# Performance work log

Hardware: AMD Instinct MI355X
Metric: run time of the kernel (lower is better)

The kernel has to match this reference:

```python
import jax, jax.numpy as jnp
import numpy as np

DIM = 192; HEADS = 6; WS = 8; OVERLAP = 2; PAD = 3; STRIDE = WS - OVERLAP; HID = DIM * 4

_coords = np.stack(np.meshgrid(np.arange(WS), np.arange(WS), indexing='ij'), 0).reshape(2, -1)
_rel = (_coords[:, :, None] - _coords[:, None, :]).transpose(1, 2, 0).astype(np.int64)
_rel[..., 0] += WS - 1; _rel[..., 1] += WS - 1; _rel[..., 0] *= 2 * WS - 1
REL_IDX = jnp.asarray(_rel.sum(-1).reshape(-1))  # (WS^2 * WS^2,)


def _ln_c(x, g, b):
    # LayerNorm over channel dim of NCHW (LayerNormProxy)
    mu = jnp.mean(x, axis=1, keepdims=True)
    var = jnp.mean((x - mu) ** 2, axis=1, keepdims=True)
    return (x - mu) * jax.lax.rsqrt(var + 1e-5) * g[:, None, None] + b[:, None, None]


def _conv1x1(x, w, b):
    return jnp.einsum('bchw,oc->bohw', x, w) + b[:, None, None]


def _dwconv3(x, w, b):
    y = jax.lax.conv_general_dilated(x, w, (1, 1), ((1, 1), (1, 1)),
                                     feature_group_count=x.shape[1],
                                     dimension_numbers=('NCHW', 'OIHW', 'NCHW'))
    return y + b[:, None, None]


def _unfold(x, k, s, p):
    # F.unfold: (B,C,H,W) -> (B, C*k*k, L) with (C,kh,kw) channel order, row-major windows
    B, C, H, W = x.shape
    xp = jnp.pad(x, ((0, 0), (0, 0), (p, p), (p, p)))
    Lh = (H + 2 * p - k) // s + 1; Lw = (W + 2 * p - k) // s + 1
    ih = (jnp.arange(Lh) * s)[:, None] + jnp.arange(k)  # (Lh,k)
    iw = (jnp.arange(Lw) * s)[:, None] + jnp.arange(k)  # (Lw,k)
    t = xp[:, :, ih, :][:, :, :, :, iw]                 # (B,C,Lh,k,Lw,k)
    t = t.transpose(0, 1, 3, 5, 2, 4)                   # (B,C,k,k,Lh,Lw)
    return t.reshape(B, C * k * k, Lh * Lw)


def _fold(cols, h, w, k, s, p):
    # F.fold: (B, C*k*k, L) -> (B,C,h,w), summing overlaps
    B = cols.shape[0]
    Lh = (h + 2 * p - k) // s + 1; Lw = (w + 2 * p - k) // s + 1
    C = cols.shape[1] // (k * k)
    t = cols.reshape(B, C, k, k, Lh, Lw).transpose(0, 1, 4, 2, 5, 3)  # (B,C,Lh,k,Lw,k)
    ih = (jnp.arange(Lh) * s)[:, None] + jnp.arange(k)
    iw = (jnp.arange(Lw) * s)[:, None] + jnp.arange(k)
    out = jnp.zeros((B, C, h + 2 * p, w + 2 * p), cols.dtype)
    out = out.at[:, :, ih[:, :, None, None], iw[None, None, :, :]].add(t)
    return out[:, :, p:p + h, p:p + w]


def _reverse(win, h, w):
    B, L, nH, ws2, ch = win.shape
    cols = win.transpose(0, 2, 4, 3, 1).reshape(B, nH * ch * ws2, L)
    return _fold(cols, h, w, WS, STRIDE, PAD)


def _hft(x, w, b):
    # HFTAttention: high-frequency residual of multi-scale avg pools, dw-conv sigmoid gate
    B, C, h, ww = x.shape
    a = 3.0 * x
    for s in (2, 4, 8):
        pool = x.reshape(B, C, h // s, s, ww // s, s).mean(axis=(3, 5))
        a = a - jnp.repeat(jnp.repeat(pool, s, axis=2), s, axis=3)
    return jax.nn.sigmoid(_dwconv3(a, w, b)) * x


def _forward(x, n1g, n1b, qkv_w, qkv_b, temp, rpb, proj_w, proj_b, hft_w, hft_b,
             n2g, n2b, fc1_w, fc1_b, sgn_g, sgn_b, sg_w, sg_b, fc2_w, fc2_b):
    B, C, H, W = x.shape
    ch = C // HEADS
    y = _conv1x1(_ln_c(x, n1g, n1b), qkv_w, qkv_b)       # (B,3C,H,W)
    cols = _unfold(y, WS, STRIDE, PAD)
    L = cols.shape[-1]
    win = cols.reshape(B, 3 * HEADS, ch, WS * WS, L).transpose(0, 4, 1, 3, 2)  # (B,L,3H,ws2,ch)
    q = win[:, :, :HEADS] * temp[None, None]
    k = win[:, :, HEADS:2 * HEADS]
    v = win[:, :, 2 * HEADS:]
    attn = jnp.einsum('blhic,blhjc->blhij', q, k)
    bias = rpb[REL_IDX].reshape(WS * WS, WS * WS, HEADS).transpose(2, 0, 1)
    attn = attn + bias[None, None]
    e = jnp.exp(attn - jnp.max(attn, axis=-1, keepdims=True))
    s = jnp.sum(e, axis=-1, keepdims=True)               # (B,L,H,ws2,1)
    s_img = _reverse(s, H, W)                            # (B,HEADS,H,W): folded softmax denom
    o = jnp.einsum('blhij,blhjc->blhic', e, v)
    o_img = _reverse(o, H, W).reshape(B, HEADS, ch, H, W)
    out = (o_img / s_img[:, :, None]).reshape(B, C, H, W)
    out = _hft(_conv1x1(out, proj_w, proj_b), hft_w, hft_b)
    x1 = x + out
    z = jax.nn.gelu(_conv1x1(_ln_c(x1, n2g, n2b), fc1_w, fc1_b), approximate=False)
    z1, z2 = jnp.split(z, 2, axis=1)
    z = z1 * _dwconv3(_ln_c(z2, sgn_g, sgn_b), sg_w, sg_b)
    return x1 + _conv1x1(z, fc2_w, fc2_b)


def setup_inputs() -> dict:
    key = jax.random.key(0)
    ks = jax.random.split(key, 8)
    B, Hi, Wi = 4, 128, 128
    f = jnp.float32
    return {
        'x': jax.random.normal(ks[0], (B, DIM, Hi, Wi), f),
        'n1g': jnp.ones((DIM,), f), 'n1b': jnp.zeros((DIM,), f),
        'qkv_w': jax.random.normal(ks[1], (3 * DIM, DIM), f) * 0.02,
        'qkv_b': jnp.zeros((3 * DIM,), f),
        'temp': jnp.ones((HEADS, 1, 1), f),
        'rpb': jax.random.normal(ks[2], ((2 * WS - 1) ** 2, HEADS), f) * 0.02,
        'proj_w': jax.random.normal(ks[3], (DIM, DIM), f) * 0.02,
        'proj_b': jnp.zeros((DIM,), f),
        'hft_w': jax.random.normal(ks[4], (DIM, 1, 3, 3), f) * 0.02,
        'hft_b': jnp.zeros((DIM,), f),
        'n2g': jnp.ones((DIM,), f), 'n2b': jnp.zeros((DIM,), f),
        'fc1_w': jax.random.normal(ks[5], (HID, DIM), f) * 0.02,
        'fc1_b': jnp.zeros((HID,), f),
        'sgn_g': jnp.ones((HID // 2,), f), 'sgn_b': jnp.zeros((HID // 2,), f),
        'sg_w': jax.random.normal(ks[6], (HID // 2, 1, 3, 3), f) * 0.02,
        'sg_b': jnp.zeros((HID // 2,), f),
        'fc2_w': jax.random.normal(ks[7], (DIM, HID // 2), f) * 0.02,
        'fc2_b': jnp.zeros((DIM,), f),
    }


def reference(x, n1g, n1b, qkv_w, qkv_b, temp, rpb, proj_w, proj_b, hft_w, hft_b,
              n2g, n2b, fc1_w, fc1_b, sgn_g, sgn_b, sg_w, sg_b, fc2_w, fc2_b):
    return _forward(x, n1g, n1b, qkv_w, qkv_b, temp, rpb, proj_w, proj_b, hft_w, hft_b,
                    n2g, n2b, fc1_w, fc1_b, sgn_g, sgn_b, sg_w, sg_b, fc2_w, fc2_b)
```

## Files before the change

kernel.cpp:

```cpp
#include <hip/hip_runtime.h>
#include <math.h>

static constexpr int B_    = 4;
static constexpr int C_    = 192;
static constexpr int NPIX  = 16384;
static constexpr int PTOT  = B_ * NPIX;
static constexpr int HEADS = 6;
static constexpr int STR   = 6;
static constexpr int LH    = 22;
static constexpr int LWIN  = LH * LH;
static constexpr int NWIN  = B_ * LWIN;

typedef short bf16x8 __attribute__((ext_vector_type(8)));
typedef float f32x4  __attribute__((ext_vector_type(4)));

__device__ __forceinline__ unsigned short f2bf(float f) {
    union { float f; unsigned int u; } v; v.f = f;
    return (unsigned short)((v.u + 0x8000u) >> 16);
}
__device__ __forceinline__ float bf2f(unsigned short h) {
    union { unsigned int u; float f; } v; v.u = ((unsigned int)h) << 16;
    return v.f;
}
__device__ __forceinline__ unsigned int pack2bf(float a, float b) {
    union { float f; unsigned int u; } x, y; x.f = a; y.f = b;
    return __builtin_amdgcn_perm(y.u + 0x8000u, x.u + 0x8000u, 0x07060302u);
}
__device__ __forceinline__ float gelu_f(float v) {
    float vv = v * v;
    float u  = v * fmaf(vv, 0.0713548162f, 1.5957691216f);
    float ue = (u > 80.f) ? 80.f : u;
    float e  = __expf(ue);
    float r  = __builtin_amdgcn_rcpf(e + 1.f);
    return v * e * r;
}

__global__ __launch_bounds__(256) void prep_k(const float* __restrict__ W, const float* __restrict__ g,
                                              const float* __restrict__ bln, const float* __restrict__ bias,
                                              int M, int K,
                                              unsigned short* __restrict__ wgb, float* __restrict__ wsum,
                                              float* __restrict__ wb) {
    int o = blockIdx.x * 256 + threadIdx.x;
    if (o >= M) return;
    float sum = 0.f, bb = 0.f;
    for (int c = 0; c < K; ++c) {
        float wv = W[(size_t)o * K + c];
        float wgv = wv * g[c];
        wgb[(size_t)o * K + c] = f2bf(wgv);
        sum += wgv;
        bb += wv * bln[c];
    }
    wsum[o] = sum;
    wb[o] = bb + bias[o];
}

__global__ __launch_bounds__(256) void wcvt_k(const float* __restrict__ W, unsigned short* __restrict__ Wb, int n) {
    int i = blockIdx.x * 256 + threadIdx.x;
    if (i < n) Wb[i] = f2bf(W[i]);
}

__global__ __launch_bounds__(256) void lnstats_z2_k(const unsigned short* __restrict__ z,
                                                    float* __restrict__ mu, float* __restrict__ rs) {
    __shared__ float red[2][4][64];
    int n0 = blockIdx.x << 6, b = blockIdx.y;
    int t = threadIdx.x;
    int px = n0 + (t & 63), cg = t >> 6;
    float s = 0.f, s2 = 0.f;
    for (int c = cg; c < 384; c += 4) {
        float v = bf2f(z[((size_t)(b * 768 + 384 + c) << 14) + px]);
        s += v; s2 += v * v;
    }
    red[0][cg][t & 63] = s;
    red[1][cg][t & 63] = s2;
    __syncthreads();
    if (t < 64) {
        float ss  = red[0][0][t] + red[0][1][t] + red[0][2][t] + red[0][3][t];
        float ss2 = red[1][0][t] + red[1][1][t] + red[1][2][t] + red[1][3][t];
        float m = ss * (1.f / 384.f);
        mu[(b << 14) + n0 + t] = m;
        rs[(b << 14) + n0 + t] = rsqrtf(ss2 * (1.f / 384.f) - m * m + 1e-5f);
    }
}

template <int KK, int INMODE, int MPB, int ACT, bool LN, bool RES, bool OBF>
__global__ __launch_bounds__(256) void gemm4_k(const unsigned short* __restrict__ Wb,
                                               const void* __restrict__ Xin,
                                               void* __restrict__ outv,
                                               const float* __restrict__ wsum, const float* __restrict__ wb,
                                               const float* __restrict__ resid, int M, int bstride) {
    constexpr int LDK     = KK + 8;
    constexpr int KSTEPS  = KK / 32;
    constexpr int PFG     = (KSTEPS > 6) ? 6 : KSTEPS;
    __shared__ unsigned short xs[64 * LDK];
    __shared__ float sred[2][4][64];
    __shared__ float muL[64], rsL[64];

    int t = threadIdx.x;
    int pt = blockIdx.x;
    int b  = pt >> 8;
    int n0 = (pt & 255) << 6;

    if constexpr (INMODE == 0) {
        const unsigned short* xg = (const unsigned short*)Xin + (size_t)(b * NPIX + n0) * KK;
        constexpr int NJ = KK / 8;
        #pragma unroll
        for (int i = 0; i < 64 * NJ / 256; ++i) {
            int c = i * 256 + t;
            int p, j;
            if (KK == 192) { p = (c * 2731) >> 16; j = c - p * 24; }
            else           { int q = c >> 4; p = (q * 21846) >> 16; j = c - p * 48; }
            uint4 v = *(const uint4*)(xg + (size_t)c * 8);
            *(uint4*)&xs[p * LDK + j * 8] = v;
        }
    } else if constexpr (INMODE == 1) {
        const float* xg = (const float*)Xin + (size_t)b * bstride + n0;
        int px = t & 63, c0 = t >> 6;
        float s = 0.f, s2 = 0.f;
        #pragma unroll 4
        for (int st = 0; st < KK / 4; ++st) {
            int c = c0 + 4 * st;
            float v = xg[(size_t)c * NPIX + px];
            s += v; s2 += v * v;
            xs[px * LDK + c] = f2bf(v);
        }
        sred[0][c0][px] = s;
        sred[1][c0][px] = s2;
        __syncthreads();
        if (t < 64) {
            float ss  = sred[0][0][t] + sred[0][1][t] + sred[0][2][t] + sred[0][3][t];
            float ss2 = sred[1][0][t] + sred[1][1][t] + sred[1][2][t] + sred[1][3][t];
            float m = ss * (1.f / (float)KK);
            muL[t] = m;
            rsL[t] = rsqrtf(ss2 * (1.f / (float)KK) - m * m + 1e-5f);
        }
    } else {
        const unsigned short* xg = (const unsigned short*)Xin + (size_t)b * bstride + n0;
        int px2 = (t & 31) << 1, c0 = t >> 5;
        #pragma unroll 4
        for (int st = 0; st < KK / 8; ++st) {
            int c = c0 + 8 * st;
            unsigned int v = *(const unsigned int*)(xg + (size_t)c * NPIX + px2);
            xs[px2 * LDK + c]       = (unsigned short)(v & 0xFFFFu);
            xs[(px2 + 1) * LDK + c] = (unsigned short)(v >> 16);
        }
    }
    __syncthreads();

    int w  = t >> 6, l = t & 63;
    int wr = w >> 1, wc = w & 1;
    int lr = l & 15, kb = l >> 4;
    int pw = wr * 32;

    bf16x8 afr[KSTEPS][2];
    #pragma unroll
    for (int ks = 0; ks < KSTEPS; ++ks)
        #pragma unroll
        for (int m = 0; m < 2; ++m)
            afr[ks][m] = *(const bf16x8*)&xs[(pw + m * 16 + lr) * LDK + ks * 32 + kb * 8];

    float rsv[2][4], murs[2][4];
    if (LN) {
        #pragma unroll
        for (int m = 0; m < 2; ++m) {
            int pl = pw + m * 16 + kb * 4;
            #pragma unroll
            for (int r = 0; r < 4; ++r) {
                float mv = muL[pl + r];
                rsv[m][r] = rsL[pl + r];
                murs[m][r] = mv * rsv[m][r];
            }
        }
    }

    int ocbase = blockIdx.y * MPB;
    #pragma unroll 2
    for (int oc = 0; oc < MPB; ++oc) {
        int ow = ((ocbase + oc) << 6) + wc * 32;
        f32x4 acc[2][2];
        #pragma unroll
        for (int m = 0; m < 2; ++m)
            #pragma unroll
            for (int n = 0; n < 2; ++n) acc[m][n] = (f32x4){0.f, 0.f, 0.f, 0.f};

        #pragma unroll
        for (int kg = 0; kg < KSTEPS; kg += PFG) {
            bf16x8 bfr[PFG][2];
            #pragma unroll
            for (int kk = 0; kk < PFG; ++kk)
                #pragma unroll
                for (int n = 0; n < 2; ++n)
                    bfr[kk][n] = *(const bf16x8*)(Wb + (size_t)(ow + n * 16 + lr) * KK + (kg + kk) * 32 + kb * 8);
            #pragma unroll
            for (int kk = 0; kk < PFG; ++kk)
                #pragma unroll
                for (int m = 0; m < 2; ++m)
                    #pragma unroll
                    for (int n = 0; n < 2; ++n)
                        acc[m][n] = __builtin_amdgcn_mfma_f32_16x16x32_bf16(afr[kg + kk][m], bfr[kk][n], acc[m][n], 0, 0, 0);
        }

        #pragma unroll
        for (int m = 0; m < 2; ++m) {
            int nidx = n0 + pw + m * 16 + kb * 4;
            #pragma unroll
            for (int n = 0; n < 2; ++n) {
                int o = ow + n * 16 + lr;
                float wbv = wb[o];
                float wsv = 0.f; if (LN) wsv = wsum[o];
                size_t obase = (((size_t)b * M + o) << 14) + nidx;
                float rv[4] = {0.f, 0.f, 0.f, 0.f};
                if (RES) {
                    float4 rr = *(const float4*)(resid + obase);
                    rv[0] = rr.x; rv[1] = rr.y; rv[2] = rr.z; rv[3] = rr.w;
                }
                float vo[4];
                #pragma unroll
                for (int r = 0; r < 4; ++r) {
                    float a = acc[m][n][r];
                    float v;
                    if (LN) { float t1 = fmaf(-murs[m][r], wsv, wbv); v = fmaf(rsv[m][r], a, t1); }
                    else    v = a + wbv;
                    if (ACT == 1) v = gelu_f(v);
                    vo[r] = v + rv[r];
                }
                if (OBF) {
                    uint2 u;
                    u.x = pack2bf(vo[0], vo[1]);
                    u.y = pack2bf(vo[2], vo[3]);
                    *(uint2*)((unsigned short*)outv + obase) = u;
                } else {
                    float4 f = {vo[0], vo[1], vo[2], vo[3]};
                    *(float4*)((float*)outv + obase) = f;
                }
            }
        }
    }
}

__global__ __launch_bounds__(64) void attn_mfma_k(const unsigned short* __restrict__ qkv,
                                                  const float* __restrict__ rpb,
                                                  const float* __restrict__ temp,
                                                  unsigned short* __restrict__ o_win,
                                                  float* __restrict__ s_win) {
    __shared__ unsigned short p_lds[64 * 72];
    __shared__ float rp[225];
    int wh = blockIdx.x;
    int head = wh % HEADS;
    int bw = wh / HEADS;
    int b = bw / LWIN, l = bw % LWIN;
    int sh = l / LH, sw = l % LH;
    int h0 = sh * STR - 3, w0 = sw * STR - 3;
    int t = threadIdx.x;
    int lr = t & 15, kb = t >> 4;

    for (int i = t; i < 225; i += 64) rp[i] = rpb[i * HEADS + head];
    float tmp = temp[head];

    const size_t qbase = ((size_t)(b * 576 + head * 32)) << 14;
    const unsigned short* qp = qkv + qbase;
    const unsigned short* kp = qkv + qbase + ((size_t)192 << 14);
    const unsigned short* vp = qkv + qbase + ((size_t)384 << 14);

    bf16x8 kf[4], qf[4];
    #pragma unroll
    for (int m = 0; m < 4; ++m) {
        int jp = m * 16 + lr;
        int hh = h0 + (jp >> 3), ww = w0 + (jp & 7);
        bool ok = ((unsigned)hh < 128u) && ((unsigned)ww < 128u);
        int pix = (hh << 7) + ww;
        #pragma unroll
        for (int j = 0; j < 8; ++j) {
            unsigned short kv = 0, qv = 0;
            if (ok) {
                size_t off = ((size_t)(kb * 8 + j) << 14) + pix;
                kv = kp[off];
                qv = qp[off];
            }
            kf[m][j] = (short)kv;
            qf[m][j] = (short)qv;
        }
    }

    f32x4 st[4][4];
    #pragma unroll
    for (int m = 0; m < 4; ++m)
        #pragma unroll
        for (int n = 0; n < 4; ++n) st[m][n] = (f32x4){0.f, 0.f, 0.f, 0.f};
    #pragma unroll
    for (int m = 0; m < 4; ++m)
        #pragma unroll
        for (int n = 0; n < 4; ++n)
            st[m][n] = __builtin_amdgcn_mfma_f32_16x16x32_bf16(kf[m], qf[n], st[m][n], 0, 0, 0);

    bf16x8 vf[2][2];
    #pragma unroll
    for (int np = 0; np < 2; ++np) {
        #pragma unroll
        for (int ks = 0; ks < 2; ++ks) {
            int hh = h0 + ks * 4 + kb;
            bool okr = (unsigned)hh < 128u;
            const unsigned short* vrow = vp + (((size_t)(np * 16 + lr)) << 14) + (hh << 7) + w0;
            #pragma unroll
            for (int j = 0; j < 8; ++j) {
                int ww = w0 + j;
                unsigned short vv = 0;
                if (okr && (unsigned)ww < 128u) vv = vrow[j];
                vf[np][ks][j] = (short)vv;
            }
        }
    }

    __syncthreads();

    #pragma unroll
    for (int n = 0; n < 4; ++n) {
        int i = n * 16 + lr;
        int iyy = i >> 3, ixx = i & 7;
        #pragma unroll
        for (int m = 0; m < 4; ++m) {
            #pragma unroll
            for (int r = 0; r < 4; ++r) {
                int j = m * 16 + kb * 4 + r;
                int dy = iyy - (j >> 3) + 7;
                int dx = ixx - (j & 7) + 7;
                st[m][n][r] = st[m][n][r] * tmp + rp[dy * 15 + dx];
            }
        }
    }

    #pragma unroll
    for (int n = 0; n < 4; ++n) {
        float mx = -1e30f;
        #pragma unroll
        for (int m = 0; m < 4; ++m)
            #pragma unroll
            for (int r = 0; r < 4; ++r) mx = fmaxf(mx, st[m][n][r]);
        mx = fmaxf(mx, __shfl_xor(mx, 16));
        mx = fmaxf(mx, __shfl_xor(mx, 32));
        float s = 0.f;
        #pragma unroll
        for (int m = 0; m < 4; ++m) {
            #pragma unroll
            for (int r = 0; r < 4; ++r) {
                float e = __expf(st[m][n][r] - mx);
                st[m][n][r] = e;
                s += e;
            }
        }
        s += __shfl_xor(s, 16);
        s += __shfl_xor(s, 32);
        int i = n * 16 + lr;
        if (kb == 0) s_win[(size_t)wh * 64 + i] = s;
        #pragma unroll
        for (int m = 0; m < 4; ++m) {
            *(unsigned int*)&p_lds[i * 72 + m * 16 + kb * 4]     = pack2bf(st[m][n][0], st[m][n][1]);
            *(unsigned int*)&p_lds[i * 72 + m * 16 + kb * 4 + 2] = pack2bf(st[m][n][2], st[m][n][3]);
        }
    }

    __syncthreads();

    f32x4 oc[4][2];
    #pragma unroll
    for (int m = 0; m < 4; ++m)
        #pragma unroll
        for (int np = 0; np < 2; ++np) oc[m][np] = (f32x4){0.f, 0.f, 0.f, 0.f};
    #pragma unroll
    for (int ks = 0; ks < 2; ++ks) {
        bf16x8 pa[4];
        #pragma unroll
        for (int m = 0; m < 4; ++m)
            pa[m] = *(const bf16x8*)&p_lds[(m * 16 + lr) * 72 + ks * 32 + kb * 8];
        #pragma unroll
        for (int m = 0; m < 4; ++m)
            #pragma unroll
            for (int np = 0; np < 2; ++np)
                oc[m][np] = __builtin_amdgcn_mfma_f32_16x16x32_bf16(pa[m], vf[np][ks], oc[m][np], 0, 0, 0);
    }

    unsigned short* ob = o_win + (size_t)wh * 2048;
    #pragma unroll
    for (int m = 0; m < 4; ++m) {
        int ibase = m * 16 + kb * 4;
        #pragma unroll
        for (int np = 0; np < 2; ++np) {
            int c = np * 16 + lr;
            #pragma unroll
            for (int r = 0; r < 4; ++r)
                ob[(ibase + r) * 32 + c] = f2bf(oc[m][np][r]);
        }
    }
}

__device__ __forceinline__ void win_range(int h, int& s0, int& s1) {
    s0 = (h + 1) / 6; if (s0 < 0) s0 = 0;
    s1 = (h + 3) / 6; if (s1 > 21) s1 = 21;
}

__global__ __launch_bounds__(256) void simg_k(const float* __restrict__ s_win, float* __restrict__ s_img) {
    int tid = blockIdx.x * 256 + threadIdx.x;
    if (tid >= B_ * HEADS * NPIX) return;
    int n = tid & (NPIX - 1);
    int bh = tid >> 14;
    int hd = bh % HEADS, b = bh / HEADS;
    int hy = n >> 7, wx = n & 127;
    int sy0, sy1, sx0, sx1;
    win_range(hy, sy0, sy1);
    win_range(wx, sx0, sx1);
    float acc = 0.f;
    for (int sy = sy0; sy <= sy1; ++sy)
        for (int sx = sx0; sx <= sx1; ++sx) {
            int idx = (hy - (sy * 6 - 3)) * 8 + (wx - (sx * 6 - 3));
            acc += s_win[(size_t)((b * LWIN + sy * LH + sx) * HEADS + hd) * 64 + idx];
        }
    s_img[tid] = acc;
}

__global__ __launch_bounds__(256) void fold_k(const unsigned short* __restrict__ o_win,
                                              const float* __restrict__ s_img,
                                              unsigned short* __restrict__ attn_t) {
    int tid = blockIdx.x * 256 + threadIdx.x;
    int q = (int)((((unsigned long long)(tid >> 3)) * 174763ull) >> 19);
    int oct = tid - q * 24;
    int n = q & (NPIX - 1), b = q >> 14;
    int hd = oct >> 2, c8 = (oct & 3) << 3;
    int hy = n >> 7, wx = n & 127;
    int sy0, sy1, sx0, sx1;
    win_range(hy, sy0, sy1);
    win_range(wx, sx0, sx1);
    float acc[8] = {0.f, 0.f, 0.f, 0.f, 0.f, 0.f, 0.f, 0.f};
    for (int sy = sy0; sy <= sy1; ++sy)
        for (int sx = sx0; sx <= sx1; ++sx) {
            int idx = (hy - (sy * 6 - 3)) * 8 + (wx - (sx * 6 - 3));
            const unsigned short* p = o_win + ((size_t)((b * LWIN + sy * LH + sx) * HEADS + hd) * 2048 + idx * 32 + c8);
            uint4 v = *(const uint4*)p;
            unsigned int arr[4] = {v.x, v.y, v.z, v.w};
            #pragma unroll
            for (int j = 0; j < 4; ++j) {
                acc[2 * j]     += bf2f((unsigned short)(arr[j] & 0xFFFFu));
                acc[2 * j + 1] += bf2f((unsigned short)(arr[j] >> 16));
            }
        }
    float inv = __builtin_amdgcn_rcpf(s_img[((b * HEADS + hd) << 14) + n]);
    unsigned int pk[4];
    #pragma unroll
    for (int j = 0; j < 4; ++j)
        pk[j] = pack2bf(acc[2 * j] * inv, acc[2 * j + 1] * inv);
    *(uint4*)&attn_t[((size_t)((b << 14) + n)) * 192 + hd * 32 + c8] = make_uint4(pk[0], pk[1], pk[2], pk[3]);
}

template <typename TI>
__global__ __launch_bounds__(256) void halve_k(const TI* __restrict__ in, float* __restrict__ out, int Win) {
    int Wo = Win >> 1;
    int tot = B_ * C_ * Wo * Wo;
    int tid = blockIdx.x * 256 + threadIdx.x;
    if (tid >= tot) return;
    int xy = tid % (Wo * Wo);
    int bc = tid / (Wo * Wo);
    int y = xy / Wo, x = xy % Wo;
    const TI* p = in + (size_t)bc * Win * Win + (size_t)(2 * y) * Win + 2 * x;
    float a, bq, c, d;
    if constexpr (sizeof(TI) == 2) {
        a = bf2f(p[0]); bq = bf2f(p[1]); c = bf2f(p[Win]); d = bf2f(p[Win + 1]);
    } else {
        a = p[0]; bq = p[1]; c = p[Win]; d = p[Win + 1];
    }
    out[tid] = 0.25f * (a + bq + c + d);
}

__global__ __launch_bounds__(256) void hft_fused_k(const unsigned short* __restrict__ po, const float* __restrict__ x,
                                                   const float* __restrict__ p2, const float* __restrict__ p4,
                                                   const float* __restrict__ p8, const float* __restrict__ hw,
                                                   const float* __restrict__ hb, float* __restrict__ x1) {
    __shared__ float tile[34 * 133];
    int rt = blockIdx.x, ch = blockIdx.y, b = blockIdx.z;
    int bc = b * C_ + ch;
    int y0 = rt << 5;
    int t = threadIdx.x;
    const unsigned short* pob = po + ((size_t)bc << 14);
    const float* p2b = p2 + ((size_t)bc << 12);
    const float* p4b = p4 + ((size_t)bc << 10);
    const float* p8b = p8 + ((size_t)bc << 8);

    for (int idx = t; idx < 34 * 133; idx += 256) {
        int row = idx / 133, col = idx - row * 133;
        int yy = y0 + row - 1, xw = col - 1;
        float val = 0.f;
        if (col < 130 && (unsigned)yy < 128u && (unsigned)xw < 128u) {
            int nn = (yy << 7) + xw;
            val = 3.f * bf2f(pob[nn])
                - p2b[((yy >> 1) << 6) + (xw >> 1)]
                - p4b[((yy >> 2) << 5) + (xw >> 2)]
                - p8b[((yy >> 3) << 4) + (xw >> 3)];
        }
        tile[idx] = val;
    }
    __syncthreads();

    float wv[9];
    #pragma unroll
    for (int k = 0; k < 9; ++k) wv[k] = hw[ch * 9 + k];
    float hbv = hb[ch];

    int r = t & 31, c0 = (t >> 5) << 4;
    int nbase = ((y0 + r) << 7) + c0;
    const float* xb = x + ((size_t)bc << 14);
    float* x1b = x1 + ((size_t)bc << 14);

    float pov[16], xv[16];
    {
        const uint4* pp4 = (const uint4*)(pob + nbase);
        uint4 a0 = pp4[0], a1 = pp4[1];
        unsigned int arr[8] = {a0.x, a0.y, a0.z, a0.w, a1.x, a1.y, a1.z, a1.w};
        #pragma unroll
        for (int j = 0; j < 8; ++j) {
            pov[2 * j]     = bf2f((unsigned short)(arr[j] & 0xFFFFu));
            pov[2 * j + 1] = bf2f((unsigned short)(arr[j] >> 16));
        }
        #pragma unroll
        for (int j4 = 0; j4 < 4; ++j4) {
            float4 xx = *(const float4*)(xb + nbase + 4 * j4);
            xv[4*j4] = xx.x; xv[4*j4+1] = xx.y; xv[4*j4+2] = xx.z; xv[4*j4+3] = xx.w;
        }
    }
    float res[16];
    #pragma unroll
    for (int j = 0; j < 16; ++j) {
        float acc = hbv;
        #pragma unroll
        for (int dy = 0; dy < 3; ++dy)
            #pragma unroll
            for (int dx = 0; dx < 3; ++dx)
                acc += wv[dy * 3 + dx] * tile[(r + dy) * 133 + c0 + j + dx];
        float sg = __builtin_amdgcn_rcpf(1.f + __expf(-acc));
        res[j] = xv[j] + sg * pov[j];
    }
    #pragma unroll
    for (int j4 = 0; j4 < 4; ++j4) {
        float4 o = {res[4*j4], res[4*j4+1], res[4*j4+2], res[4*j4+3]};
        *(float4*)(x1b + nbase + 4 * j4) = o;
    }
}

__global__ __launch_bounds__(256) void sgmul_k(unsigned short* __restrict__ z,
                                               const float* __restrict__ mu3, const float* __restrict__ rs3,
                                               const float* __restrict__ sgn_g, const float* __restrict__ sgn_b,
                                               const float* __restrict__ sg_w, const float* __restrict__ sg_b) {
    __shared__ float tile[34 * 133];
    int rt = blockIdx.x, ch = blockIdx.y, b = blockIdx.z;
    int y0 = rt << 5;
    int t = threadIdx.x;
    const unsigned short* zb = z + ((size_t)(b * 768 + 384 + ch) << 14);
    unsigned short* z1p = z + ((size_t)(b * 768 + ch) << 14);
    const float* mub = mu3 + (b << 14);
    const float* rsb = rs3 + (b << 14);
    float g = sgn_g[ch], bb = sgn_b[ch];

    for (int idx = t; idx < 34 * 133; idx += 256) {
        int row = idx / 133, col = idx - row * 133;
        int yy = y0 + row - 1, xw = col - 1;
        float val = 0.f;
        if (col < 130 && (unsigned)yy < 128u && (unsigned)xw < 128u) {
            int nn = (yy << 7) + xw;
            val = (bf2f(zb[nn]) - mub[nn]) * rsb[nn] * g + bb;
        }
        tile[idx] = val;
    }
    __syncthreads();

    float wv[9];
    #pragma unroll
    for (int k = 0; k < 9; ++k) wv[k] = sg_w[ch * 9 + k];
    float sb = sg_b[ch];

    int r = t & 31, c0 = (t >> 5) << 4;
    int nbase = ((y0 + r) << 7) + c0;

    float res[16];
    #pragma unroll
    for (int j = 0; j < 16; ++j) {
        float acc = sb;
        #pragma unroll
        for (int dy = 0; dy < 3; ++dy)
            #pragma unroll
            for (int dx = 0; dx < 3; ++dx)
                acc += wv[dy * 3 + dx] * tile[(r + dy) * 133 + c0 + j + dx];
        res[j] = acc;
    }
    uint4* zp = (uint4*)(z1p + nbase);
    uint4 v0 = zp[0], v1 = zp[1];
    unsigned int arr[8] = {v0.x, v0.y, v0.z, v0.w, v1.x, v1.y, v1.z, v1.w};
    #pragma unroll
    for (int j = 0; j < 8; ++j) {
        float lo = bf2f((unsigned short)(arr[j] & 0xFFFFu)) * res[2 * j];
        float hi = bf2f((unsigned short)(arr[j] >> 16)) * res[2 * j + 1];
        arr[j] = pack2bf(lo, hi);
    }
    zp[0] = make_uint4(arr[0], arr[1], arr[2], arr[3]);
    zp[1] = make_uint4(arr[4], arr[5], arr[6], arr[7]);
}

extern "C" void kernel_launch(void* const* d_in, const int* in_sizes, int n_in,
                              void* d_out, int out_size, void* d_ws, size_t ws_size,
                              hipStream_t stream) {
    const float* x     = (const float*)d_in[0];
    const float* n1g   = (const float*)d_in[1];
    const float* n1b   = (const float*)d_in[2];
    const float* qkv_w = (const float*)d_in[3];
    const float* qkv_b = (const float*)d_in[4];
    const float* temp  = (const float*)d_in[5];
    const float* rpb   = (const float*)d_in[6];
    const float* proj_w= (const float*)d_in[7];
    const float* proj_b= (const float*)d_in[8];
    const float* hft_w = (const float*)d_in[9];
    const float* hft_b = (const float*)d_in[10];
    const float* n2g   = (const float*)d_in[11];
    const float* n2b   = (const float*)d_in[12];
    const float* fc1_w = (const float*)d_in[13];
    const float* fc1_b = (const float*)d_in[14];
    const float* sgn_g = (const float*)d_in[15];
    const float* sgn_b = (const float*)d_in[16];
    const float* sg_w  = (const float*)d_in[17];
    const float* sg_b  = (const float*)d_in[18];
    const float* fc2_w = (const float*)d_in[19];
    const float* fc2_b = (const float*)d_in[20];
    float* out = (float*)d_out;
    float* w = (float*)d_ws;

    float* mu3 = w + 262144;   float* rs3 = w + 327680;
    unsigned short* wgb_qkv = (unsigned short*)(w + 393216);
    float* wsum_qkv = w + 448512;  float* wb_qkv = w + 449088;
    unsigned short* wgb_fc1 = (unsigned short*)(w + 449664);
    float* wsum_fc1 = w + 523392;  float* wb_fc1 = w + 524160;
    unsigned short* pwb  = (unsigned short*)(w + 524928);
    unsigned short* f2wb = (unsigned short*)(w + 543360);
    unsigned short* attn_t = (unsigned short*)(w + 580224);
    unsigned short* qkvb = (unsigned short*)(w + 6871680);
    unsigned short* proj_out = (unsigned short*)(w + 6871680);
    float* p2 = w + 19454592;  float* p4 = w + 22600320;  float* p8 = w + 23386752;
    unsigned short* o_win = (unsigned short*)(w + 25746048);
    float* s_win = w + 49535616;
    float* s_img = w + 50279040;
    unsigned short* z = (unsigned short*)(w + 25746048);
    float* x1 = w + 50911872;

    prep_k<<<3, 256, 0, stream>>>(qkv_w, n1g, n1b, qkv_b, 576, 192, wgb_qkv, wsum_qkv, wb_qkv);
    gemm4_k<192, 1, 9, 0, true, false, true><<<dim3(1024, 1), 256, 0, stream>>>(
        wgb_qkv, x, qkvb, wsum_qkv, wb_qkv, nullptr, 576, 192 * NPIX);
    attn_mfma_k<<<NWIN * HEADS, 64, 0, stream>>>(qkvb, rpb, temp, o_win, s_win);
    simg_k<<<1536, 256, 0, stream>>>(s_win, s_img);
    fold_k<<<6144, 256, 0, stream>>>(o_win, s_img, attn_t);
    wcvt_k<<<144, 256, 0, stream>>>(proj_w, pwb, 192 * 192);
    gemm4_k<192, 0, 1, 0, false, false, true><<<dim3(1024, 3), 256, 0, stream>>>(
        pwb, attn_t, proj_out, nullptr, proj_b, nullptr, 192, 0);
    halve_k<unsigned short><<<12288, 256, 0, stream>>>(proj_out, p2, 128);
    halve_k<float><<<3072, 256, 0, stream>>>(p2, p4, 64);
    halve_k<float><<<768, 256, 0, stream>>>(p4, p8, 32);
    hft_fused_k<<<dim3(4, 192, B_), 256, 0, stream>>>(proj_out, x, p2, p4, p8, hft_w, hft_b, x1);
    prep_k<<<3, 256, 0, stream>>>(fc1_w, n2g, n2b, fc1_b, 768, 192, wgb_fc1, wsum_fc1, wb_fc1);
    gemm4_k<192, 1, 12, 1, true, false, true><<<dim3(1024, 1), 256, 0, stream>>>(
        wgb_fc1, x1, z, wsum_fc1, wb_fc1, nullptr, 768, 192 * NPIX);
    lnstats_z2_k<<<dim3(256, B_), 256, 0, stream>>>(z, mu3, rs3);
    sgmul_k<<<dim3(4, 384, B_), 256, 0, stream>>>(z, mu3, rs3, sgn_g, sgn_b, sg_w, sg_b);
    wcvt_k<<<288, 256, 0, stream>>>(fc2_w, f2wb, 192 * 384);
    gemm4_k<384, 2, 3, 0, false, true, false><<<dim3(1024, 1), 256, 0, stream>>>(
        f2wb, z, out, nullptr, fc2_b, x1, 192, 768 * NPIX);
}
```

Before: 628.8 us.

## Fuse fold into projection GEMM and compute LN stats in fc1 epilogue

Replaces the separate fold kernel and the projection GEMM with one kernel. It gathers the overlapping window outputs into LDS and runs the MFMA projection directly, so the attn_t intermediate never goes through global memory. It also removes the separate lnstats pass by accumulating per-pixel sum and sum-of-squares of the second half of the fc1 output in the GEMM epilogue. The trade-off is a projection kernel with 1024 blocks instead of 3072, and extra registers, shuffles and a sync in the fc1 GEMM.

```diff
diff --git a/kernel.cpp b/kernel.cpp
--- a/kernel.cpp
+++ b/kernel.cpp
@@ -59,35 +59,13 @@
     if (i < n) Wb[i] = f2bf(W[i]);
 }
 
-__global__ __launch_bounds__(256) void lnstats_z2_k(const unsigned short* __restrict__ z,
-                                                    float* __restrict__ mu, float* __restrict__ rs) {
-    __shared__ float red[2][4][64];
-    int n0 = blockIdx.x << 6, b = blockIdx.y;
-    int t = threadIdx.x;
-    int px = n0 + (t & 63), cg = t >> 6;
-    float s = 0.f, s2 = 0.f;
-    for (int c = cg; c < 384; c += 4) {
-        float v = bf2f(z[((size_t)(b * 768 + 384 + c) << 14) + px]);
-        s += v; s2 += v * v;
-    }
-    red[0][cg][t & 63] = s;
-    red[1][cg][t & 63] = s2;
-    __syncthreads();
-    if (t < 64) {
-        float ss  = red[0][0][t] + red[0][1][t] + red[0][2][t] + red[0][3][t];
-        float ss2 = red[1][0][t] + red[1][1][t] + red[1][2][t] + red[1][3][t];
-        float m = ss * (1.f / 384.f);
-        mu[(b << 14) + n0 + t] = m;
-        rs[(b << 14) + n0 + t] = rsqrtf(ss2 * (1.f / 384.f) - m * m + 1e-5f);
-    }
-}
-
-template <int KK, int INMODE, int MPB, int ACT, bool LN, bool RES, bool OBF>
+template <int KK, int INMODE, int MPB, int ACT, bool LN, bool RES, bool OBF, int STATS>
 __global__ __launch_bounds__(256) void gemm4_k(const unsigned short* __restrict__ Wb,
                                                const void* __restrict__ Xin,
                                                void* __restrict__ outv,
                                                const float* __restrict__ wsum, const float* __restrict__ wb,
-                                               const float* __restrict__ resid, int M, int bstride) {
+                                               const float* __restrict__ resid, int M, int bstride,
+                                               float* __restrict__ smu, float* __restrict__ srs) {
     constexpr int LDK     = KK + 8;
     constexpr int KSTEPS  = KK / 32;
     constexpr int PFG     = (KSTEPS > 6) ? 6 : KSTEPS;
@@ -170,6 +148,14 @@
                 murs[m][r] = mv * rsv[m][r];
             }
         }
+    }
+
+    float zs[2][4], zs2[2][4];
+    if constexpr (STATS) {
+        #pragma unroll
+        for (int m = 0; m < 2; ++m)
+            #pragma unroll
+            for (int r = 0; r < 4; ++r) { zs[m][r] = 0.f; zs2[m][r] = 0.f; }
     }
 
     int ocbase = blockIdx.y * MPB;
@@ -222,6 +208,9 @@
                     else    v = a + wbv;
                     if (ACT == 1) v = gelu_f(v);
                     vo[r] = v + rv[r];
+                    if constexpr (STATS) {
+                        if (oc >= MPB / 2) { zs[m][r] += vo[r]; zs2[m][r] += vo[r] * vo[r]; }
+                    }
                 }
                 if (OBF) {
                     uint2 u;
@@ -233,6 +222,31 @@
                     *(float4*)((float*)outv + obase) = f;
                 }
             }
+        }
+    }
+
+    if constexpr (STATS) {
+        __shared__ float sst[64][2][2];
+        #pragma unroll
+        for (int m = 0; m < 2; ++m)
+            #pragma unroll
+            for (int r = 0; r < 4; ++r) {
+                float a  = zs[m][r], c2 = zs2[m][r];
+                a  += __shfl_xor(a, 1);  a  += __shfl_xor(a, 2);  a  += __shfl_xor(a, 4);  a  += __shfl_xor(a, 8);
+                c2 += __shfl_xor(c2, 1); c2 += __shfl_xor(c2, 2); c2 += __shfl_xor(c2, 4); c2 += __shfl_xor(c2, 8);
+                if (lr == 0) {
+                    int pp = pw + m * 16 + kb * 4 + r;
+                    sst[pp][wc][0] = a; sst[pp][wc][1] = c2;
+                }
+            }
+        __syncthreads();
+        if (t < 64) {
+            float ss  = sst[t][0][0] + sst[t][1][0];
+            float ss2 = sst[t][0][1] + sst[t][1][1];
+            float invC = 2.f / (float)M;
+            float mm = ss * invC;
+            smu[(b << 14) + n0 + t] = mm;
+            srs[(b << 14) + n0 + t] = rsqrtf(ss2 * invC - mm * mm + 1e-5f);
         }
     }
 }
@@ -416,37 +430,105 @@
     s_img[tid] = acc;
 }
 
-__global__ __launch_bounds__(256) void fold_k(const unsigned short* __restrict__ o_win,
-                                              const float* __restrict__ s_img,
-                                              unsigned short* __restrict__ attn_t) {
-    int tid = blockIdx.x * 256 + threadIdx.x;
-    int q = (int)((((unsigned long long)(tid >> 3)) * 174763ull) >> 19);
-    int oct = tid - q * 24;
-    int n = q & (NPIX - 1), b = q >> 14;
-    int hd = oct >> 2, c8 = (oct & 3) << 3;
-    int hy = n >> 7, wx = n & 127;
-    int sy0, sy1, sx0, sx1;
-    win_range(hy, sy0, sy1);
-    win_range(wx, sx0, sx1);
-    float acc[8] = {0.f, 0.f, 0.f, 0.f, 0.f, 0.f, 0.f, 0.f};
-    for (int sy = sy0; sy <= sy1; ++sy)
-        for (int sx = sx0; sx <= sx1; ++sx) {
-            int idx = (hy - (sy * 6 - 3)) * 8 + (wx - (sx * 6 - 3));
-            const unsigned short* p = o_win + ((size_t)((b * LWIN + sy * LH + sx) * HEADS + hd) * 2048 + idx * 32 + c8);
-            uint4 v = *(const uint4*)p;
-            unsigned int arr[4] = {v.x, v.y, v.z, v.w};
-            #pragma unroll
-            for (int j = 0; j < 4; ++j) {
-                acc[2 * j]     += bf2f((unsigned short)(arr[j] & 0xFFFFu));
-                acc[2 * j + 1] += bf2f((unsigned short)(arr[j] >> 16));
-            }
-        }
-    float inv = __builtin_amdgcn_rcpf(s_img[((b * HEADS + hd) << 14) + n]);
-    unsigned int pk[4];
-    #pragma unroll
-    for (int j = 0; j < 4; ++j)
-        pk[j] = pack2bf(acc[2 * j] * inv, acc[2 * j + 1] * inv);
-    *(uint4*)&attn_t[((size_t)((b << 14) + n)) * 192 + hd * 32 + c8] = make_uint4(pk[0], pk[1], pk[2], pk[3]);
+__global__ __launch_bounds__(256) void fold_proj_k(const unsigned short* __restrict__ o_win,
+                                                   const float* __restrict__ s_img,
+                                                   const unsigned short* __restrict__ Wb,
+                                                   const float* __restrict__ wb,
+                                                   unsigned short* __restrict__ outv) {
+    constexpr int KK = 192, LDK = 200, KSTEPS = 6, PFG = 6, MPB = 3;
+    __shared__ unsigned short xs[64 * LDK];
+
+    int t = threadIdx.x;
+    int pt = blockIdx.x;
+    int b  = pt >> 8;
+    int n0 = (pt & 255) << 6;
+
+    #pragma unroll
+    for (int it = 0; it < 6; ++it) {
+        int item = it * 256 + t;
+        int px = (item * 2731) >> 16;
+        int oct = item - px * 24;
+        int n = n0 + px;
+        int hd = oct >> 2, c8 = (oct & 3) << 3;
+        int hy = n >> 7, wx = n & 127;
+        int sy0, sy1, sx0, sx1;
+        win_range(hy, sy0, sy1);
+        win_range(wx, sx0, sx1);
+        float acc[8] = {0.f, 0.f, 0.f, 0.f, 0.f, 0.f, 0.f, 0.f};
+        for (int sy = sy0; sy <= sy1; ++sy)
+            for (int sx = sx0; sx <= sx1; ++sx) {
+                int idx = (hy - (sy * 6 - 3)) * 8 + (wx - (sx * 6 - 3));
+                const unsigned short* p = o_win + ((size_t)((b * LWIN + sy * LH + sx) * HEADS + hd) * 2048 + idx * 32 + c8);
+                uint4 v = *(const uint4*)p;
+                unsigned int arr[4] = {v.x, v.y, v.z, v.w};
+                #pragma unroll
+                for (int j = 0; j < 4; ++j) {
+                    acc[2 * j]     += bf2f((unsigned short)(arr[j] & 0xFFFFu));
+                    acc[2 * j + 1] += bf2f((unsigned short)(arr[j] >> 16));
+                }
+            }
+        float inv = __builtin_amdgcn_rcpf(s_img[((b * HEADS + hd) << 14) + n]);
+        unsigned int pk[4];
+        #pragma unroll
+        for (int j = 0; j < 4; ++j)
+            pk[j] = pack2bf(acc[2 * j] * inv, acc[2 * j + 1] * inv);
+        *(uint4*)&xs[px * LDK + hd * 32 + c8] = make_uint4(pk[0], pk[1], pk[2], pk[3]);
+    }
+    __syncthreads();
+
+    int w  = t >> 6, l = t & 63;
+    int wr = w >> 1, wc = w & 1;
+    int lr = l & 15, kb = l >> 4;
+    int pw = wr * 32;
+
+    bf16x8 afr[KSTEPS][2];
+    #pragma unroll
+    for (int ks = 0; ks < KSTEPS; ++ks)
+        #pragma unroll
+        for (int m = 0; m < 2; ++m)
+            afr[ks][m] = *(const bf16x8*)&xs[(pw + m * 16 + lr) * LDK + ks * 32 + kb * 8];
+
+    #pragma unroll
+    for (int oc = 0; oc < MPB; ++oc) {
+        int ow = (oc << 6) + wc * 32;
+        f32x4 acc2[2][2];
+        #pragma unroll
+        for (int m = 0; m < 2; ++m)
+            #pragma unroll
+            for (int n = 0; n < 2; ++n) acc2[m][n] = (f32x4){0.f, 0.f, 0.f, 0.f};
+
+        #pragma unroll
+        for (int kg = 0; kg < KSTEPS; kg += PFG) {
+            bf16x8 bfr[PFG][2];
+            #pragma unroll
+            for (int kk = 0; kk < PFG; ++kk)
+                #pragma unroll
+                for (int n = 0; n < 2; ++n)
+                    bfr[kk][n] = *(const bf16x8*)(Wb + (size_t)(ow + n * 16 + lr) * KK + (kg + kk) * 32 + kb * 8);
+            #pragma unroll
+            for (int kk = 0; kk < PFG; ++kk)
+                #pragma unroll
+                for (int m = 0; m < 2; ++m)
+                    #pragma unroll
+                    for (int n = 0; n < 2; ++n)
+                        acc2[m][n] = __builtin_amdgcn_mfma_f32_16x16x32_bf16(afr[kg + kk][m], bfr[kk][n], acc2[m][n], 0, 0, 0);
+        }
+
+        #pragma unroll
+        for (int m = 0; m < 2; ++m) {
+            int nidx = n0 + pw + m * 16 + kb * 4;
+            #pragma unroll
+            for (int n = 0; n < 2; ++n) {
+                int o = ow + n * 16 + lr;
+                float wbv = wb[o];
+                size_t obase = (((size_t)b * 192 + o) << 14) + nidx;
+                uint2 u;
+                u.x = pack2bf(acc2[m][n][0] + wbv, acc2[m][n][1] + wbv);
+                u.y = pack2bf(acc2[m][n][2] + wbv, acc2[m][n][3] + wbv);
+                *(uint2*)(outv + obase) = u;
+            }
+        }
+    }
 }
 
 template <typename TI>
@@ -634,9 +716,8 @@
     float* wsum_fc1 = w + 523392;  float* wb_fc1 = w + 524160;
     unsigned short* pwb  = (unsigned short*)(w + 524928);
     unsigned short* f2wb = (unsigned short*)(w + 543360);
-    unsigned short* attn_t = (unsigned short*)(w + 580224);
     unsigned short* qkvb = (unsigned short*)(w + 6871680);
-    unsigned short* proj_out = (unsigned short*)(w + 6871680);
+    unsigned short* proj_out = (unsigned short*)(w + 580224);
     float* p2 = w + 19454592;  float* p4 = w + 22600320;  float* p8 = w + 23386752;
     unsigned short* o_win = (unsigned short*)(w + 25746048);
     float* s_win = w + 49535616;
@@ -645,24 +726,21 @@
     float* x1 = w + 50911872;
 
     prep_k<<<3, 256, 0, stream>>>(qkv_w, n1g, n1b, qkv_b, 576, 192, wgb_qkv, wsum_qkv, wb_qkv);
-    gemm4_k<192, 1, 9, 0, true, false, true><<<dim3(1024, 1), 256, 0, stream>>>(
-        wgb_qkv, x, qkvb, wsum_qkv, wb_qkv, nullptr, 576, 192 * NPIX);
+    wcvt_k<<<144, 256, 0, stream>>>(proj_w, pwb, 192 * 192);
+    gemm4_k<192, 1, 9, 0, true, false, true, 0><<<dim3(1024, 1), 256, 0, stream>>>(
+        wgb_qkv, x, qkvb, wsum_qkv, wb_qkv, nullptr, 576, 192 * NPIX, nullptr, nullptr);
     attn_mfma_k<<<NWIN * HEADS, 64, 0, stream>>>(qkvb, rpb, temp, o_win, s_win);
     simg_k<<<1536, 256, 0, stream>>>(s_win, s_img);
-    fold_k<<<6144, 256, 0, stream>>>(o_win, s_img, attn_t);
-    wcvt_k<<<144, 256, 0, stream>>>(proj_w, pwb, 192 * 192);
-    gemm4_k<192, 0, 1, 0, false, false, true><<<dim3(1024, 3), 256, 0, stream>>>(
-        pwb, attn_t, proj_out, nullptr, proj_b, nullptr, 192, 0);
+    fold_proj_k<<<1024, 256, 0, stream>>>(o_win, s_img, pwb, proj_b, proj_out);
     halve_k<unsigned short><<<12288, 256, 0, stream>>>(proj_out, p2, 128);
     halve_k<float><<<3072, 256, 0, stream>>>(p2, p4, 64);
     halve_k<float><<<768, 256, 0, stream>>>(p4, p8, 32);
     hft_fused_k<<<dim3(4, 192, B_), 256, 0, stream>>>(proj_out, x, p2, p4, p8, hft_w, hft_b, x1);
     prep_k<<<3, 256, 0, stream>>>(fc1_w, n2g, n2b, fc1_b, 768, 192, wgb_fc1, wsum_fc1, wb_fc1);
-    gemm4_k<192, 1, 12, 1, true, false, true><<<dim3(1024, 1), 256, 0, stream>>>(
-        wgb_fc1, x1, z, wsum_fc1, wb_fc1, nullptr, 768, 192 * NPIX);
-    lnstats_z2_k<<<dim3(256, B_), 256, 0, stream>>>(z, mu3, rs3);
+    gemm4_k<192, 1, 12, 1, true, false, true, 1><<<dim3(1024, 1), 256, 0, stream>>>(
+        wgb_fc1, x1, z, wsum_fc1, wb_fc1, nullptr, 768, 192 * NPIX, mu3, rs3);
     sgmul_k<<<dim3(4, 384, B_), 256, 0, stream>>>(z, mu3, rs3, sgn_g, sgn_b, sg_w, sg_b);
     wcvt_k<<<288, 256, 0, stream>>>(fc2_w, f2wb, 192 * 384);
-    gemm4_k<384, 2, 3, 0, false, true, false><<<dim3(1024, 1), 256, 0, stream>>>(
-        f2wb, z, out, nullptr, fc2_b, x1, 192, 768 * NPIX);
-}
+    gemm4_k<384, 2, 3, 0, false, true, false, 0><<<dim3(1024, 1), 256, 0, stream>>>(
+        f2wb, z, out, nullptr, fc2_b, x1, 192, 768 * NPIX, nullptr, nullptr);
+}
```

Measured after the change: 598.2 us (median of 3 runs). 4.9% less time.
